# Optimization experiments

Hardware: AMD Instinct MI355X
Metric: run time of the kernel (lower is better)

The kernel has to match this reference:

```python
import jax, jax.numpy as jnp
import numpy as np

SEQ, B = 128, 512
PT, EH, ZS, DH, NM, NMAX = 5, 256, 128, 512, 20, 256


def setup_inputs() -> dict:
    key = jax.random.key(0)
    ks = jax.random.split(key, 24)
    rn = lambda k, sh, sc=0.05: jax.random.normal(k, sh, dtype=jnp.float32) * sc
    return {
        "s": rn(ks[0], (SEQ, B, PT), 1.0),
        "enc_Wih_f": rn(ks[1], (4 * EH, PT)), "enc_Whh_f": rn(ks[2], (4 * EH, EH)), "enc_b_f": rn(ks[3], (4 * EH,)),
        "enc_Wih_b": rn(ks[4], (4 * EH, PT)), "enc_Whh_b": rn(ks[5], (4 * EH, EH)), "enc_b_b": rn(ks[6], (4 * EH,)),
        "Wmu": rn(ks[7], (ZS, 2 * EH)), "bmu": rn(ks[8], (ZS,)),
        "Wsig": rn(ks[9], (ZS, 2 * EH)), "bsig": rn(ks[10], (ZS,)),
        "Wh0": rn(ks[11], (DH, ZS)), "bh0": rn(ks[12], (DH,)),
        "dec_Wih": rn(ks[13], (4 * DH, PT + ZS)), "dec_Whh": rn(ks[14], (4 * DH, DH)), "dec_b": rn(ks[15], (4 * DH,)),
        "Wdec": rn(ks[16], (6 * NM + 3, DH)), "bdec": rn(ks[17], (6 * NM + 3,)),
        "z_eps": rn(ks[18], (B, ZS), 1.0),
        "gmm_eps": rn(ks[19], (NMAX, B, NM, 2), 1.0),
        "pen_u": jax.random.uniform(ks[20], (NMAX, B, 3), dtype=jnp.float32),
    }


def _lstm_dir(x, Wih, Whh, b, reverse):
    # PyTorch gate order: i, f, g, o. Returns final hidden state [B, H].
    H = Whh.shape[1]
    Bn = x.shape[1]
    def step(carry, xt):
        h, c = carry
        g = xt @ Wih.T + h @ Whh.T + b
        i, f, gg, o = jnp.split(g, 4, axis=-1)
        c = jax.nn.sigmoid(f) * c + jax.nn.sigmoid(i) * jnp.tanh(gg)
        h = jax.nn.sigmoid(o) * jnp.tanh(c)
        return (h, c), None
    init = (jnp.zeros((Bn, H), x.dtype), jnp.zeros((Bn, H), x.dtype))
    (h, _), _ = jax.lax.scan(step, init, x, reverse=reverse)
    return h


def reference(s, enc_Wih_f, enc_Whh_f, enc_b_f, enc_Wih_b, enc_Whh_b, enc_b_b,
              Wmu, bmu, Wsig, bsig, Wh0, bh0,
              dec_Wih, dec_Whh, dec_b, Wdec, bdec,
              z_eps, gmm_eps, pen_u):
    Bn = s.shape[1]
    # Bidirectional encoder -> concat last hidden states [B, 2*EH]
    hf = _lstm_dir(s, enc_Wih_f, enc_Whh_f, enc_b_f, False)
    hb = _lstm_dir(s, enc_Wih_b, enc_Whh_b, enc_b_b, True)
    h = jnp.concatenate([hf, hb], axis=-1)
    # Reparameterized latent
    mu = h @ Wmu.T + bmu
    sigma = jnp.exp((h @ Wsig.T + bsig) * 0.5)
    z = mu + sigma * z_eps                      # [B, ZS]
    h0 = jnp.tanh(z @ Wh0.T + bh0)              # [B, DH]
    c0 = jnp.zeros_like(h0)
    s0 = jnp.tile(jnp.array([0.0, 0.0, 1.0, 0.0, 0.0], jnp.float32), (Bn, 1))

    def step(carry, noise):
        prev, hc, cc = carry
        eps, u = noise                          # eps [B,NM,2], u [B,3]
        x = jnp.concatenate([prev, z], axis=-1)  # [B, PT+ZS]
        g = x @ dec_Wih.T + hc @ dec_Whh.T + dec_b
        i, f, gg, o = jnp.split(g, 4, axis=-1)
        cc = jax.nn.sigmoid(f) * cc + jax.nn.sigmoid(i) * jnp.tanh(gg)
        hc = jax.nn.sigmoid(o) * jnp.tanh(cc)
        y = hc @ Wdec.T + bdec                  # [B, 6*NM+3]
        mix = y[:, :6 * NM].reshape(Bn, NM, 6)
        pi = jax.nn.softmax(mix[..., 0], axis=-1)
        mx, my = mix[..., 1], mix[..., 2]
        sx, sy = jnp.exp(mix[..., 3]), jnp.exp(mix[..., 4])
        cor = jnp.tanh(mix[..., 5])
        # Sample from N(mean, [[sx^2, cor],[cor, sy^2]]) via Cholesky (cov as in source)
        l21 = cor / sx
        l22 = jnp.sqrt(jnp.maximum(sy * sy - l21 * l21, 1e-6))
        e1, e2 = eps[..., 0], eps[..., 1]
        samp_x = mx + sx * e1
        samp_y = my + l21 * e1 + l22 * e2
        dx = jnp.sum(pi * samp_x, axis=-1)      # pi-weighted sum over mixtures (as in source)
        dy = jnp.sum(pi * samp_y, axis=-1)
        q = jax.nn.softmax(y[:, -3:], axis=-1)
        pen = (u < q).astype(jnp.float32)       # independent Bernoulli thresholds, as in source
        point = jnp.concatenate([dx[:, None], dy[:, None], pen], axis=-1)
        return (point, hc, cc), point

    _, sketch = jax.lax.scan(step, (s0, h0, c0), (gmm_eps, pen_u))
    return sketch  # [NMAX, B, 5]
```

## Files before the change

kernel.cpp:

```cpp
#include <hip/hip_runtime.h>
#include <math.h>

#define B     512
#define SEQL  128
#define PT    5
#define EH    256
#define ZS    128
#define DH    512
#define NM    20
#define NMAXT 256

__device__ __forceinline__ float sigf(float x) { return 1.0f / (1.0f + expf(-x)); }

#define FMA8(m, av, lo, hi)                                                   \
    acc[m][0]=fmaf(av,lo.x,acc[m][0]); acc[m][1]=fmaf(av,lo.y,acc[m][1]);     \
    acc[m][2]=fmaf(av,lo.z,acc[m][2]); acc[m][3]=fmaf(av,lo.w,acc[m][3]);     \
    acc[m][4]=fmaf(av,hi.x,acc[m][4]); acc[m][5]=fmaf(av,hi.y,acc[m][5]);     \
    acc[m][6]=fmaf(av,hi.z,acc[m][6]); acc[m][7]=fmaf(av,hi.w,acc[m][7]);

#define XSUM(v) v += __shfl_xor(v,1); v += __shfl_xor(v,2); v += __shfl_xor(v,4); \
                v += __shfl_xor(v,8); v += __shfl_xor(v,16); v += __shfl_xor(v,32);

__global__ void transpose_pad(const float* __restrict__ in, float* __restrict__ out,
                              int rows, int cols, int rpad, long islice, long oslice)
{
    const float* ip = in + (size_t)blockIdx.z * islice;
    float* op = out + (size_t)blockIdx.z * oslice;
    int idx = blockIdx.x * 256 + threadIdx.x;
    if (idx >= cols * rpad) return;
    int c = idx / rpad, r = idx - c * rpad;
    op[idx] = (r < rows) ? ip[(size_t)r * cols + c] : 0.0f;
}

__global__ __launch_bounds__(512, 4) void enc_step4(
    const float* __restrict__ sT,
    const float* __restrict__ WihF, const float* __restrict__ WhhF, const float* __restrict__ bF,
    const float* __restrict__ WihB, const float* __restrict__ WhhB, const float* __restrict__ bB,
    const float* __restrict__ hfin, float* __restrict__ hfout, float* __restrict__ cf,
    const float* __restrict__ hbin, float* __restrict__ hbout, float* __restrict__ cb,
    int t)
{
    __shared__ float lds[17408];

    const int tid = threadIdx.x;
    const int x   = blockIdx.x;
    const int ng  = x & 31;
    const int bg  = (x >> 5) & 7;
    const int dir = x >> 8;
    const int n0  = ng * 8;
    const int b0  = bg * 64;

    const float* Whh  = dir ? WhhB : WhhF;
    const float* Wih  = dir ? WihB : WihF;
    const float* bias = dir ? bB   : bF;
    const float* hin  = dir ? hbin : hfin;
    float* hout       = dir ? hbout: hfout;
    float* c          = dir ? cb   : cf;
    const int ts = dir ? (SEQL - 1 - t) : t;

    #pragma unroll
    for (int i = 0; i < 4; ++i) {
        const int fidx = i * 512 + tid;
        const int w   = fidx >> 9;
        const int rem = fidx & 511;
        const int r   = rem >> 4, s5 = rem & 15;
        const int g   = r >> 3, nn = r & 7;
        const float4 wv4 = *(const float4*)&Whh[(size_t)(g * EH + n0 + nn) * EH + w * 64 + s5 * 4];
        *(float4*)&lds[((w * 32 + r) * 16 + (s5 ^ ((r >> 2) & 7))) * 4] = wv4;
    }
    __syncthreads();

    const int lane = tid & 63;
    const int wv   = tid >> 6;
    const int ri   = lane & 7;
    const int bi   = lane >> 3;
    const int wq   = wv >> 1;
    const int sb   = (wv & 1) * 8;
    const float* hcol = hin + b0 + bi * 8;

    float acc[4][8];
    #pragma unroll
    for (int m = 0; m < 4; ++m)
        #pragma unroll
        for (int j = 0; j < 8; ++j) acc[m][j] = 0.0f;

    #pragma unroll 2
    for (int j4 = 0; j4 < 8; ++j4) {
        float4 a[4];
        #pragma unroll
        for (int m = 0; m < 4; ++m)
            a[m] = *(const float4*)&lds[((wq * 32 + ri * 4 + m) * 16 + (sb | (j4 ^ ri))) * 4];
        const int kb = wv * 32 + j4 * 4;
        #pragma unroll
        for (int jj = 0; jj < 4; ++jj) {
            const float* hp = hcol + (size_t)(kb + jj) * B;
            const float4 blo = *(const float4*)hp;
            const float4 bhi = *(const float4*)(hp + 4);
            #pragma unroll
            for (int m = 0; m < 4; ++m) {
                const float av = (jj == 0) ? a[m].x : (jj == 1) ? a[m].y : (jj == 2) ? a[m].z : a[m].w;
                FMA8(m, av, blo, bhi)
            }
        }
    }
    __syncthreads();

    #pragma unroll
    for (int m = 0; m < 4; ++m) {
        float* pr = &lds[(wv * 32 + ri * 4 + m) * 68 + bi * 8];
        *(float4*)pr       = make_float4(acc[m][0], acc[m][1], acc[m][2], acc[m][3]);
        *(float4*)(pr + 4) = make_float4(acc[m][4], acc[m][5], acc[m][6], acc[m][7]);
    }
    __syncthreads();

    const int nn = tid & 7;
    const int c0 = tid >> 3;
    const int b  = b0 + c0;

    float ps[4];
    #pragma unroll
    for (int g = 0; g < 4; ++g) {
        const int r = g * 8 + nn;
        float v = 0.0f;
        #pragma unroll
        for (int w8 = 0; w8 < 8; ++w8) v += lds[(w8 * 32 + r) * 68 + c0];
        ps[g] = v;
    }

    const float x0 = sT[((size_t)ts * PT + 0) * B + b];
    const float x1 = sT[((size_t)ts * PT + 1) * B + b];
    const float x2 = sT[((size_t)ts * PT + 2) * B + b];
    const float x3 = sT[((size_t)ts * PT + 3) * B + b];
    const float x4 = sT[((size_t)ts * PT + 4) * B + b];
    float gv[4];
    #pragma unroll
    for (int g = 0; g < 4; ++g) {
        const int grow = g * EH + n0 + nn;
        const float* wr = Wih + (size_t)grow * PT;
        float v = ps[g] + bias[grow];
        v = fmaf(x0, wr[0], v); v = fmaf(x1, wr[1], v); v = fmaf(x2, wr[2], v);
        v = fmaf(x3, wr[3], v); v = fmaf(x4, wr[4], v);
        gv[g] = v;
    }
    const size_t idx = (size_t)(n0 + nn) * B + b;
    const float cv = sigf(gv[1]) * c[idx] + sigf(gv[0]) * tanhf(gv[2]);
    c[idx] = cv;
    hout[idx] = sigf(gv[3]) * tanhf(cv);
}

__global__ __launch_bounds__(512, 4) void dec_step4(
    const float* __restrict__ hin, float* __restrict__ hout, float* __restrict__ cT,
    const float* __restrict__ CzT, const float* __restrict__ Whh,
    const float* __restrict__ Wih, const float* __restrict__ prevPt, int t)
{
    __shared__ float lds[17408];

    const int tid = threadIdx.x;
    const int x   = blockIdx.x;
    const int ng  = x & 63;
    const int bg  = x >> 6;
    const int n0  = ng * 8;
    const int b0  = bg * 64;

    #pragma unroll
    for (int i = 0; i < 8; ++i) {
        const int fidx = i * 512 + tid;
        const int w   = fidx >> 10;
        const int rem = fidx & 1023;
        const int r   = rem >> 5, s5 = rem & 31;
        const int g   = r >> 3, nn = r & 7;
        const int sl  = (s5 & 16) | ((s5 & 15) ^ ((r >> 2) & 7));
        const float4 wv4 = *(const float4*)&Whh[(size_t)(g * DH + n0 + nn) * DH + w * 128 + s5 * 4];
        *(float4*)&lds[((w * 32 + r) * 32 + sl) * 4] = wv4;
    }
    __syncthreads();

    const int lane = tid & 63;
    const int wv   = tid >> 6;
    const int ri   = lane & 7;
    const int bi   = lane >> 3;
    const int wq   = wv >> 1;
    const int sb   = (wv & 1) * 16;
    const float* hcol = hin + b0 + bi * 8;

    float acc[4][8];
    #pragma unroll
    for (int m = 0; m < 4; ++m)
        #pragma unroll
        for (int j = 0; j < 8; ++j) acc[m][j] = 0.0f;

    #pragma unroll 2
    for (int j4 = 0; j4 < 16; ++j4) {
        float4 a[4];
        #pragma unroll
        for (int m = 0; m < 4; ++m)
            a[m] = *(const float4*)&lds[((wq * 32 + ri * 4 + m) * 32 + (sb | (j4 ^ ri))) * 4];
        const int kb = wv * 64 + j4 * 4;
        #pragma unroll
        for (int jj = 0; jj < 4; ++jj) {
            const float* hp = hcol + (size_t)(kb + jj) * B;
            const float4 blo = *(const float4*)hp;
            const float4 bhi = *(const float4*)(hp + 4);
            #pragma unroll
            for (int m = 0; m < 4; ++m) {
                const float av = (jj == 0) ? a[m].x : (jj == 1) ? a[m].y : (jj == 2) ? a[m].z : a[m].w;
                FMA8(m, av, blo, bhi)
            }
        }
    }
    __syncthreads();

    #pragma unroll
    for (int m = 0; m < 4; ++m) {
        float* pr = &lds[(wv * 32 + ri * 4 + m) * 68 + bi * 8];
        *(float4*)pr       = make_float4(acc[m][0], acc[m][1], acc[m][2], acc[m][3]);
        *(float4*)(pr + 4) = make_float4(acc[m][4], acc[m][5], acc[m][6], acc[m][7]);
    }
    __syncthreads();

    const int nn = tid & 7;
    const int c0 = tid >> 3;
    const int b  = b0 + c0;

    float ps[4];
    #pragma unroll
    for (int g = 0; g < 4; ++g) {
        const int r = g * 8 + nn;
        float v = 0.0f;
        #pragma unroll
        for (int w8 = 0; w8 < 8; ++w8) v += lds[(w8 * 32 + r) * 68 + c0];
        ps[g] = v;
    }

    float p0, p1, p2, p3, p4;
    if (t == 0) { p0 = 0.f; p1 = 0.f; p2 = 1.f; p3 = 0.f; p4 = 0.f; }
    else {
        const float* pp = &prevPt[(size_t)b * 5];
        p0 = pp[0]; p1 = pp[1]; p2 = pp[2]; p3 = pp[3]; p4 = pp[4];
    }
    float gv[4];
    #pragma unroll
    for (int g = 0; g < 4; ++g) {
        const int grow = g * DH + n0 + nn;
        const float* wr = Wih + (size_t)grow * 133;
        float v = ps[g] + CzT[(size_t)grow * B + b];
        v = fmaf(p0, wr[0], v); v = fmaf(p1, wr[1], v); v = fmaf(p2, wr[2], v);
        v = fmaf(p3, wr[3], v); v = fmaf(p4, wr[4], v);
        gv[g] = v;
    }
    const size_t idx = (size_t)(n0 + nn) * B + b;
    const float cv = sigf(gv[1]) * cT[idx] + sigf(gv[0]) * tanhf(gv[2]);
    cT[idx] = cv;
    hout[idx] = sigf(gv[3]) * tanhf(cv);
}

__global__ __launch_bounds__(512) void ysamp5(
    const float* __restrict__ hT, const float* __restrict__ WdecT,
    const float* __restrict__ bdec,
    const float* __restrict__ geps, const float* __restrict__ penu,
    float* __restrict__ out, int t)
{
    __shared__ float part[4][128];
    __shared__ float Y[128];

    const int tid = threadIdx.x;
    const int col = tid & 127;
    const int ks  = tid >> 7;
    const int b   = blockIdx.x;

    float a0 = 0.f;
    const float* wp = WdecT + (size_t)ks * 128 * 128 + col;
    const float* hp = hT + (size_t)ks * 128 * B + b;
    #pragma unroll 8
    for (int k = 0; k < 128; ++k)
        a0 = fmaf(wp[(size_t)k * 128], hp[(size_t)k * B], a0);
    part[ks][col] = a0;
    __syncthreads();
    if (ks == 0)
        Y[col] = part[0][col] + part[1][col] + part[2][col] + part[3][col]
               + ((col < 123) ? bdec[col] : 0.0f);
    __syncthreads();

    if (tid < 64) {
        const int lane = tid;
        const float* y = Y;
        const int m = lane;
        float pv = (m < NM) ? y[6 * m] : -1e30f;
        float mm = pv;
        mm = fmaxf(mm, __shfl_xor(mm, 1));  mm = fmaxf(mm, __shfl_xor(mm, 2));
        mm = fmaxf(mm, __shfl_xor(mm, 4));  mm = fmaxf(mm, __shfl_xor(mm, 8));
        mm = fmaxf(mm, __shfl_xor(mm, 16)); mm = fmaxf(mm, __shfl_xor(mm, 32));
        float pe = 0.f, tx = 0.f, ty = 0.f;
        if (m < NM) {
            pe = expf(pv - mm);
            const float mx = y[6 * m + 1], my = y[6 * m + 2];
            const float sx = expf(y[6 * m + 3]), sy = expf(y[6 * m + 4]);
            const float cor = tanhf(y[6 * m + 5]);
            const float l21 = cor / sx;
            const float l22 = sqrtf(fmaxf(sy * sy - l21 * l21, 1e-6f));
            const float* ep = &geps[(((size_t)t * B) + b) * (NM * 2) + 2 * m];
            const float e1 = ep[0], e2 = ep[1];
            tx = pe * fmaf(sx, e1, mx);
            ty = pe * (my + fmaf(l21, e1, l22 * e2));
        }
        XSUM(pe) XSUM(tx) XSUM(ty)
        if (lane == 0) {
            const float q0 = y[120], q1 = y[121], q2 = y[122];
            const float qm = fmaxf(q0, fmaxf(q1, q2));
            const float e0 = expf(q0 - qm), e1q = expf(q1 - qm), e2q = expf(q2 - qm);
            const float qs = e0 + e1q + e2q;
            const float* u = &penu[(((size_t)t * B) + b) * 3];
            float* o = &out[(((size_t)t * B) + b) * 5];
            o[0] = tx / pe;
            o[1] = ty / pe;
            o[2] = (u[0] < e0  / qs) ? 1.f : 0.f;
            o[3] = (u[1] < e1q / qs) ? 1.f : 0.f;
            o[4] = (u[2] < e2q / qs) ? 1.f : 0.f;
        }
    }
}

__global__ __launch_bounds__(256) void latent2(
    const float* __restrict__ hfT, const float* __restrict__ hbT,
    const float* __restrict__ Wmu, const float* __restrict__ bmu,
    const float* __restrict__ Wsig, const float* __restrict__ bsig,
    const float* __restrict__ zepsT, float* __restrict__ zT)
{
    const int lane = threadIdx.x & 63;
    const int wv   = __builtin_amdgcn_readfirstlane(threadIdx.x >> 6);
    const int b    = blockIdx.x * 64 + lane;
    const int n0   = blockIdx.y * 8 + wv * 2;

    float am[2] = {}, as2[2] = {};
    #pragma unroll 4
    for (int k0 = 0; k0 < 2 * EH; k0 += 4) {
        const float* hsrc = (k0 < EH) ? hfT : hbT;
        const int kk = k0 & (EH - 1);
        const float a0 = hsrc[(size_t)(kk + 0) * B + b];
        const float a1 = hsrc[(size_t)(kk + 1) * B + b];
        const float a2 = hsrc[(size_t)(kk + 2) * B + b];
        const float a3 = hsrc[(size_t)(kk + 3) * B + b];
        #pragma unroll
        for (int j = 0; j < 2; ++j) {
            const float4 wm = *(const float4*)&Wmu[((size_t)(n0 + j)) * (2 * EH) + k0];
            const float4 ws = *(const float4*)&Wsig[((size_t)(n0 + j)) * (2 * EH) + k0];
            float u = am[j], v = as2[j];
            u = fmaf(a0, wm.x, u); u = fmaf(a1, wm.y, u); u = fmaf(a2, wm.z, u); u = fmaf(a3, wm.w, u);
            v = fmaf(a0, ws.x, v); v = fmaf(a1, ws.y, v); v = fmaf(a2, ws.z, v); v = fmaf(a3, ws.w, v);
            am[j] = u; as2[j] = v;
        }
    }
    #pragma unroll
    for (int j = 0; j < 2; ++j) {
        const int n = n0 + j;
        const float mu = am[j] + bmu[n];
        const float sg = expf(0.5f * (as2[j] + bsig[n]));
        zT[(size_t)n * B + b] = fmaf(sg, zepsT[(size_t)n * B + b], mu);
    }
}

__global__ __launch_bounds__(256) void h02(
    const float* __restrict__ zT, const float* __restrict__ Wh0,
    const float* __restrict__ bh0, float* __restrict__ hT)
{
    const int lane = threadIdx.x & 63;
    const int wv   = __builtin_amdgcn_readfirstlane(threadIdx.x >> 6);
    const int b    = blockIdx.x * 64 + lane;
    const int n0   = blockIdx.y * 32 + wv * 8;

    float acc[8] = {};
    #pragma unroll 2
    for (int k0 = 0; k0 < ZS; k0 += 4) {
        const float a0 = zT[(size_t)(k0 + 0) * B + b];
        const float a1 = zT[(size_t)(k0 + 1) * B + b];
        const float a2 = zT[(size_t)(k0 + 2) * B + b];
        const float a3 = zT[(size_t)(k0 + 3) * B + b];
        #pragma unroll
        for (int r = 0; r < 8; ++r) {
            const float4 w = *(const float4*)&Wh0[((size_t)(n0 + r)) * ZS + k0];
            float v = acc[r];
            v = fmaf(a0, w.x, v); v = fmaf(a1, w.y, v);
            v = fmaf(a2, w.z, v); v = fmaf(a3, w.w, v);
            acc[r] = v;
        }
    }
    #pragma unroll
    for (int r = 0; r < 8; ++r)
        hT[(size_t)(n0 + r) * B + b] = tanhf(acc[r] + bh0[n0 + r]);
}

__global__ __launch_bounds__(256) void cz2(
    const float* __restrict__ zT, const float* __restrict__ Wih,
    const float* __restrict__ bias, float* __restrict__ CzT)
{
    const int lane = threadIdx.x & 63;
    const int wv   = __builtin_amdgcn_readfirstlane(threadIdx.x >> 6);
    const int b    = blockIdx.x * 64 + lane;
    const int r0   = blockIdx.y * 32 + wv * 8;

    float acc[8] = {};
    #pragma unroll 4
    for (int k = 0; k < ZS; ++k) {
        const float a = zT[(size_t)k * B + b];
        #pragma unroll
        for (int r = 0; r < 8; ++r)
            acc[r] = fmaf(a, Wih[(size_t)(r0 + r) * 133 + 5 + k], acc[r]);
    }
    #pragma unroll
    for (int r = 0; r < 8; ++r)
        CzT[(size_t)(r0 + r) * B + b] = acc[r] + bias[r0 + r];
}

extern "C" void kernel_launch(void* const* d_in, const int* in_sizes, int n_in,
                              void* d_out, int out_size, void* d_ws, size_t ws_size,
                              hipStream_t stream)
{
    (void)in_sizes; (void)n_in; (void)out_size; (void)ws_size;

    const float* s      = (const float*)d_in[0];
    const float* WihF   = (const float*)d_in[1];
    const float* WhhF   = (const float*)d_in[2];
    const float* bF     = (const float*)d_in[3];
    const float* WihB   = (const float*)d_in[4];
    const float* WhhB   = (const float*)d_in[5];
    const float* bB     = (const float*)d_in[6];
    const float* Wmu    = (const float*)d_in[7];
    const float* bmu    = (const float*)d_in[8];
    const float* Wsig   = (const float*)d_in[9];
    const float* bsig   = (const float*)d_in[10];
    const float* Wh0    = (const float*)d_in[11];
    const float* bh0    = (const float*)d_in[12];
    const float* decWih = (const float*)d_in[13];
    const float* decWhh = (const float*)d_in[14];
    const float* decB   = (const float*)d_in[15];
    const float* Wdec   = (const float*)d_in[16];
    const float* bdec   = (const float*)d_in[17];
    const float* zeps   = (const float*)d_in[18];
    const float* geps   = (const float*)d_in[19];
    const float* penu   = (const float*)d_in[20];

    float* out = (float*)d_out;
    float* p   = (float*)d_ws;

    float* hf0  = p; p += 131072;
    float* hb0  = p; p += 131072;
    float* cf   = p; p += 131072;
    float* cb   = p; p += 131072;
    float* cdT  = p; p += 262144;
    float* hf1  = p; p += 131072;
    float* hb1  = p; p += 131072;
    float* hA   = p; p += 262144;
    float* hB   = p; p += 262144;
    float* zT   = p; p += 65536;
    float* CzT  = p; p += 1048576;
    float* zepsT= p; p += 65536;
    float* WdecT= p; p += 65536;
    float* sT   = p; p += 327680;

    hipMemsetAsync((void*)hf0, 0, (size_t)(4 * 131072 + 262144) * sizeof(float), stream);

    transpose_pad<<<dim3(256, 1, 1), 256, 0, stream>>>(zeps, zepsT, B, ZS, B, 0, 0);
    transpose_pad<<<dim3(256, 1, 1), 256, 0, stream>>>(Wdec, WdecT, 123, DH, 128, 0, 0);
    transpose_pad<<<dim3(10, 1, SEQL), 256, 0, stream>>>(s, sT, B, PT, B, (long)B * PT, (long)B * PT);

    for (int t = 0; t < SEQL; ++t) {
        const float* hfin = (t & 1) ? hf1 : hf0;  float* hfout = (t & 1) ? hf0 : hf1;
        const float* hbin = (t & 1) ? hb1 : hb0;  float* hbout = (t & 1) ? hb0 : hb1;
        enc_step4<<<dim3(512), 512, 0, stream>>>(
            sT, WihF, WhhF, bF, WihB, WhhB, bB,
            hfin, hfout, cf, hbin, hbout, cb, t);
    }
    latent2<<<dim3(8, 16), 256, 0, stream>>>(hf0, hb0, Wmu, bmu, Wsig, bsig, zepsT, zT);
    h02<<<dim3(8, 16), 256, 0, stream>>>(zT, Wh0, bh0, hA);
    cz2<<<dim3(8, 64), 256, 0, stream>>>(zT, decWih, decB, CzT);

    for (int t = 0; t < NMAXT; ++t) {
        const float* hin = (t & 1) ? hB : hA;
        float* hout      = (t & 1) ? hA : hB;
        dec_step4<<<dim3(512), 512, 0, stream>>>(
            hin, hout, cdT, CzT, decWhh, decWih,
            t ? (out + (size_t)(t - 1) * B * 5) : out, t);
        ysamp5<<<dim3(512), 512, 0, stream>>>(hout, WdecT, bdec, geps, penu, out, t);
    }
}
```

Baseline: 11.07 ms.

## Prefetch epilogue operands early in LSTM steps and batch four rows per ysamp block

The encoder and decoder step kernels now load the old cell state, the inputs and the Cz terms at kernel start, so these global loads overlap the Whh staging and the matmul instead of sitting in the epilogue. The output/sampling kernel now handles four batch rows per block. It stages their hidden vectors in LDS so each Wdec weight load is reused four times, and it launches a quarter as many blocks. This reduces repeated global weight traffic and uncoalesced hidden-state reads, but leaves fewer blocks to spread across the GPU.

```diff
diff --git a/kernel.cpp b/kernel.cpp
--- a/kernel.cpp
+++ b/kernel.cpp
@@ -32,7 +32,7 @@
     op[idx] = (r < rows) ? ip[(size_t)r * cols + c] : 0.0f;
 }
 
-__global__ __launch_bounds__(512, 4) void enc_step4(
+__global__ __launch_bounds__(512, 4) void enc_step5(
     const float* __restrict__ sT,
     const float* __restrict__ WihF, const float* __restrict__ WhhF, const float* __restrict__ bF,
     const float* __restrict__ WihB, const float* __restrict__ WhhB, const float* __restrict__ bB,
@@ -57,6 +57,17 @@
     float* hout       = dir ? hbout: hfout;
     float* c          = dir ? cb   : cf;
     const int ts = dir ? (SEQL - 1 - t) : t;
+
+    const int pn = tid & 7;
+    const int pc = tid >> 3;
+    const int pb = b0 + pc;
+    const size_t pidx = (size_t)(n0 + pn) * B + pb;
+    const float cold = c[pidx];
+    const float x0 = sT[((size_t)ts * PT + 0) * B + pb];
+    const float x1 = sT[((size_t)ts * PT + 1) * B + pb];
+    const float x2 = sT[((size_t)ts * PT + 2) * B + pb];
+    const float x3 = sT[((size_t)ts * PT + 3) * B + pb];
+    const float x4 = sT[((size_t)ts * PT + 4) * B + pb];
 
     #pragma unroll
     for (int i = 0; i < 4; ++i) {
@@ -113,42 +124,32 @@
     }
     __syncthreads();
 
-    const int nn = tid & 7;
-    const int c0 = tid >> 3;
-    const int b  = b0 + c0;
-
     float ps[4];
     #pragma unroll
     for (int g = 0; g < 4; ++g) {
-        const int r = g * 8 + nn;
+        const int r = g * 8 + pn;
         float v = 0.0f;
         #pragma unroll
-        for (int w8 = 0; w8 < 8; ++w8) v += lds[(w8 * 32 + r) * 68 + c0];
+        for (int w8 = 0; w8 < 8; ++w8) v += lds[(w8 * 32 + r) * 68 + pc];
         ps[g] = v;
     }
 
-    const float x0 = sT[((size_t)ts * PT + 0) * B + b];
-    const float x1 = sT[((size_t)ts * PT + 1) * B + b];
-    const float x2 = sT[((size_t)ts * PT + 2) * B + b];
-    const float x3 = sT[((size_t)ts * PT + 3) * B + b];
-    const float x4 = sT[((size_t)ts * PT + 4) * B + b];
     float gv[4];
     #pragma unroll
     for (int g = 0; g < 4; ++g) {
-        const int grow = g * EH + n0 + nn;
+        const int grow = g * EH + n0 + pn;
         const float* wr = Wih + (size_t)grow * PT;
         float v = ps[g] + bias[grow];
         v = fmaf(x0, wr[0], v); v = fmaf(x1, wr[1], v); v = fmaf(x2, wr[2], v);
         v = fmaf(x3, wr[3], v); v = fmaf(x4, wr[4], v);
         gv[g] = v;
     }
-    const size_t idx = (size_t)(n0 + nn) * B + b;
-    const float cv = sigf(gv[1]) * c[idx] + sigf(gv[0]) * tanhf(gv[2]);
-    c[idx] = cv;
-    hout[idx] = sigf(gv[3]) * tanhf(cv);
-}
-
-__global__ __launch_bounds__(512, 4) void dec_step4(
+    const float cv = sigf(gv[1]) * cold + sigf(gv[0]) * tanhf(gv[2]);
+    c[pidx] = cv;
+    hout[pidx] = sigf(gv[3]) * tanhf(cv);
+}
+
+__global__ __launch_bounds__(512, 4) void dec_step5(
     const float* __restrict__ hin, float* __restrict__ hout, float* __restrict__ cT,
     const float* __restrict__ CzT, const float* __restrict__ Whh,
     const float* __restrict__ Wih, const float* __restrict__ prevPt, int t)
@@ -161,6 +162,22 @@
     const int bg  = x >> 6;
     const int n0  = ng * 8;
     const int b0  = bg * 64;
+
+    const int pn = tid & 7;
+    const int pc = tid >> 3;
+    const int pb = b0 + pc;
+    const size_t pidx = (size_t)(n0 + pn) * B + pb;
+    const float cold = cT[pidx];
+    float p0, p1, p2, p3, p4;
+    if (t == 0) { p0 = 0.f; p1 = 0.f; p2 = 1.f; p3 = 0.f; p4 = 0.f; }
+    else {
+        const float* pp = &prevPt[(size_t)pb * 5];
+        p0 = pp[0]; p1 = pp[1]; p2 = pp[2]; p3 = pp[3]; p4 = pp[4];
+    }
+    float cz[4];
+    #pragma unroll
+    for (int g = 0; g < 4; ++g)
+        cz[g] = CzT[(size_t)(g * DH + n0 + pn) * B + pb];
 
     #pragma unroll
     for (int i = 0; i < 8; ++i) {
@@ -218,72 +235,75 @@
     }
     __syncthreads();
 
-    const int nn = tid & 7;
-    const int c0 = tid >> 3;
-    const int b  = b0 + c0;
-
     float ps[4];
     #pragma unroll
     for (int g = 0; g < 4; ++g) {
-        const int r = g * 8 + nn;
+        const int r = g * 8 + pn;
         float v = 0.0f;
         #pragma unroll
-        for (int w8 = 0; w8 < 8; ++w8) v += lds[(w8 * 32 + r) * 68 + c0];
+        for (int w8 = 0; w8 < 8; ++w8) v += lds[(w8 * 32 + r) * 68 + pc];
         ps[g] = v;
     }
 
-    float p0, p1, p2, p3, p4;
-    if (t == 0) { p0 = 0.f; p1 = 0.f; p2 = 1.f; p3 = 0.f; p4 = 0.f; }
-    else {
-        const float* pp = &prevPt[(size_t)b * 5];
-        p0 = pp[0]; p1 = pp[1]; p2 = pp[2]; p3 = pp[3]; p4 = pp[4];
-    }
     float gv[4];
     #pragma unroll
     for (int g = 0; g < 4; ++g) {
-        const int grow = g * DH + n0 + nn;
+        const int grow = g * DH + n0 + pn;
         const float* wr = Wih + (size_t)grow * 133;
-        float v = ps[g] + CzT[(size_t)grow * B + b];
+        float v = ps[g] + cz[g];
         v = fmaf(p0, wr[0], v); v = fmaf(p1, wr[1], v); v = fmaf(p2, wr[2], v);
         v = fmaf(p3, wr[3], v); v = fmaf(p4, wr[4], v);
         gv[g] = v;
     }
-    const size_t idx = (size_t)(n0 + nn) * B + b;
-    const float cv = sigf(gv[1]) * cT[idx] + sigf(gv[0]) * tanhf(gv[2]);
-    cT[idx] = cv;
-    hout[idx] = sigf(gv[3]) * tanhf(cv);
-}
-
-__global__ __launch_bounds__(512) void ysamp5(
+    const float cv = sigf(gv[1]) * cold + sigf(gv[0]) * tanhf(gv[2]);
+    cT[pidx] = cv;
+    hout[pidx] = sigf(gv[3]) * tanhf(cv);
+}
+
+__global__ __launch_bounds__(512) void ysamp6(
     const float* __restrict__ hT, const float* __restrict__ WdecT,
     const float* __restrict__ bdec,
     const float* __restrict__ geps, const float* __restrict__ penu,
     float* __restrict__ out, int t)
 {
-    __shared__ float part[4][128];
-    __shared__ float Y[128];
+    __shared__ float h_s[512][4];
+    __shared__ float part[4][128][4];
+    __shared__ float Y[4][128];
 
     const int tid = threadIdx.x;
     const int col = tid & 127;
     const int ks  = tid >> 7;
-    const int b   = blockIdx.x;
-
-    float a0 = 0.f;
+    const int b0  = blockIdx.x * 4;
+
+    *(float4*)&h_s[tid][0] = *(const float4*)&hT[(size_t)tid * B + b0];
+    __syncthreads();
+
+    float a0 = 0.f, a1 = 0.f, a2 = 0.f, a3 = 0.f;
     const float* wp = WdecT + (size_t)ks * 128 * 128 + col;
-    const float* hp = hT + (size_t)ks * 128 * B + b;
     #pragma unroll 8
-    for (int k = 0; k < 128; ++k)
-        a0 = fmaf(wp[(size_t)k * 128], hp[(size_t)k * B], a0);
-    part[ks][col] = a0;
-    __syncthreads();
-    if (ks == 0)
-        Y[col] = part[0][col] + part[1][col] + part[2][col] + part[3][col]
-               + ((col < 123) ? bdec[col] : 0.0f);
-    __syncthreads();
-
-    if (tid < 64) {
-        const int lane = tid;
-        const float* y = Y;
+    for (int k = 0; k < 128; ++k) {
+        const float w = wp[(size_t)k * 128];
+        const float4 hq = *(const float4*)&h_s[ks * 128 + k][0];
+        a0 = fmaf(w, hq.x, a0); a1 = fmaf(w, hq.y, a1);
+        a2 = fmaf(w, hq.z, a2); a3 = fmaf(w, hq.w, a3);
+    }
+    part[ks][col][0] = a0; part[ks][col][1] = a1;
+    part[ks][col][2] = a2; part[ks][col][3] = a3;
+    __syncthreads();
+    if (ks == 0) {
+        const float bd = (col < 123) ? bdec[col] : 0.0f;
+        #pragma unroll
+        for (int j = 0; j < 4; ++j)
+            Y[j][col] = part[0][col][j] + part[1][col][j] + part[2][col][j]
+                      + part[3][col][j] + bd;
+    }
+    __syncthreads();
+
+    if (tid < 256) {
+        const int bp   = tid >> 6;
+        const int lane = tid & 63;
+        const int b    = b0 + bp;
+        const float* y = Y[bp];
         const int m = lane;
         float pv = (m < NM) ? y[6 * m] : -1e30f;
         float mm = pv;
@@ -466,7 +486,7 @@
     for (int t = 0; t < SEQL; ++t) {
         const float* hfin = (t & 1) ? hf1 : hf0;  float* hfout = (t & 1) ? hf0 : hf1;
         const float* hbin = (t & 1) ? hb1 : hb0;  float* hbout = (t & 1) ? hb0 : hb1;
-        enc_step4<<<dim3(512), 512, 0, stream>>>(
+        enc_step5<<<dim3(512), 512, 0, stream>>>(
             sT, WihF, WhhF, bF, WihB, WhhB, bB,
             hfin, hfout, cf, hbin, hbout, cb, t);
     }
@@ -477,9 +497,9 @@
     for (int t = 0; t < NMAXT; ++t) {
         const float* hin = (t & 1) ? hB : hA;
         float* hout      = (t & 1) ? hA : hB;
-        dec_step4<<<dim3(512), 512, 0, stream>>>(
+        dec_step5<<<dim3(512), 512, 0, stream>>>(
             hin, hout, cdT, CzT, decWhh, decWih,
             t ? (out + (size_t)(t - 1) * B * 5) : out, t);
-        ysamp5<<<dim3(512), 512, 0, stream>>>(hout, WdecT, bdec, geps, penu, out, t);
-    }
-}
+        ysamp6<<<dim3(128), 512, 0, stream>>>(hout, WdecT, bdec, geps, penu, out, t);
+    }
+}
```

Result: faster. 9.942 ms (-10.2%).
